# Optimization experiments

Hardware: AMD Instinct MI355X
Metric: run time of the kernel (lower is better)

Reference implementation:

```python
import jax, jax.numpy as jnp
import numpy as np

B = 2048            # reactions per batch
NODES_PER_MOL = 32
N = B * NODES_PER_MOL   # 65536 nodes per slot graph
E = 2 * N               # 131072 edges per slot graph
NODE_IN, EDGE_IN, H = 64, 16, 300
DEPTH = 3


def setup_inputs() -> dict:
    key = jax.random.key(0)
    ks = jax.random.split(key, 24)
    d = {}
    for i, s in enumerate(["r1", "r2", "p1"]):
        d[f"x_{s}"] = jax.random.normal(ks[4 * i], (N, NODE_IN), jnp.float32)
        d[f"e_{s}"] = jax.random.normal(ks[4 * i + 1], (E, EDGE_IN), jnp.float32)
        d[f"src_{s}"] = jax.random.randint(ks[4 * i + 2], (E,), 0, N, jnp.int32)
        d[f"dst_{s}"] = jax.random.randint(ks[4 * i + 3], (E,), 0, N, jnp.int32)
        d[f"seg_{s}"] = jnp.repeat(jnp.arange(B, dtype=jnp.int32), NODES_PER_MOL)
    s = 0.05
    d["Wn"] = jax.random.normal(ks[12], (NODE_IN, H), jnp.float32) * s
    d["bn"] = jnp.zeros((H,), jnp.float32)
    d["We"] = jax.random.normal(ks[13], (EDGE_IN, H), jnp.float32) * s
    d["be"] = jnp.zeros((H,), jnp.float32)
    d["W1"] = jax.random.normal(ks[14], (DEPTH, H, H), jnp.float32) * s
    d["b1"] = jnp.zeros((DEPTH, H), jnp.float32)
    d["W2"] = jax.random.normal(ks[15], (DEPTH, H, H), jnp.float32) * s
    d["b2"] = jnp.zeros((DEPTH, H), jnp.float32)
    return d


def _gin(x, e, src, dst, Wn, bn, We, be, W1, b1, W2, b2):
    # project_node_feats = Linear + ReLU ; project_edge_feats = Linear
    h = jax.nn.relu(x @ Wn + bn)           # [N, H]
    eh = e @ We + be                        # [E, H]
    n = x.shape[0]
    for l in range(DEPTH):
        # GINEConv (eps=0): agg = sum_{j->i} relu(h_j + e_ji); h = MLP(h + agg)
        m = jax.nn.relu(h[src] + eh)        # [E, H]
        agg = jax.ops.segment_sum(m, dst, num_segments=n)
        z = h + agg
        z = jax.nn.relu(z @ W1[l] + b1[l]) @ W2[l] + b2[l]
        if l < DEPTH - 1:
            z = jax.nn.relu(z)              # inter-layer ReLU (dropout = eval no-op)
        h = z
    return h


def reference(x_r1, e_r1, src_r1, dst_r1, seg_r1,
              x_r2, e_r2, src_r2, dst_r2, seg_r2,
              x_p1, e_p1, src_p1, dst_p1, seg_p1,
              Wn, bn, We, be, W1, b1, W2, b2):
    def pooled(x, e, src, dst, seg):
        h = _gin(x, e, src, dst, Wn, bn, We, be, W1, b1, W2, b2)
        # per-molecule sum pooling == the original ragged start:end slice + sum loop
        return jax.ops.segment_sum(h, seg, num_segments=B)   # [B, H]
    reactants = pooled(x_r1, e_r1, src_r1, dst_r1, seg_r1) + \
                pooled(x_r2, e_r2, src_r2, dst_r2, seg_r2)
    products = pooled(x_p1, e_p1, src_p1, dst_p1, seg_p1)
    reaction_feat = reactants - products
    return (reaction_feat, reactants, products)
```

## Files before the change

### kernel.cpp

```cpp
#include <hip/hip_runtime.h>

typedef _Float16 half8 __attribute__((ext_vector_type(8)));
typedef _Float16 half4 __attribute__((ext_vector_type(4)));
typedef float    f32x4 __attribute__((ext_vector_type(4)));

#define N_NODES 65536
#define N_EDGES 131072
#define BB      2048
#define HDIM    300
#define HPAD    320

__global__ __launch_bounds__(256) void prepack_w(const float* __restrict__ src,
                                                 _Float16* __restrict__ dst,
                                                 int Kpad, int Kreal) {
    int idx = blockIdx.x * 256 + threadIdx.x;
    int n = idx / Kpad, k = idx - n * Kpad;
    if (n >= 384) return;
    float v = (n < 300 && k < Kreal) ? src[k * 300 + n] : 0.f;
    dst[idx] = (_Float16)v;
}

__global__ __launch_bounds__(256) void cvt_x(const float* __restrict__ x,
                                             _Float16* __restrict__ xh, int n) {
    int i = blockIdx.x * 256 + threadIdx.x;
    if (i < n) xh[i] = (_Float16)x[i];
}

__global__ __launch_bounds__(256) void cvt_e_csr(const float* __restrict__ ein,
                                                 const int2* __restrict__ se,
                                                 _Float16* __restrict__ ecsr) {
    int i = blockIdx.x * 256 + threadIdx.x;
    if (i >= N_EDGES * 32) return;
    int k = i & 31, s = i >> 5;
    int e = se[s].y;
    ecsr[i] = (_Float16)(k < 16 ? ein[(size_t)e * 16 + k] : 0.f);
}

__device__ __forceinline__ void gload16(const _Float16* g, _Float16* l) {
    __builtin_amdgcn_global_load_lds(
        (const __attribute__((address_space(1))) void*)g,
        (__attribute__((address_space(3))) void*)l, 16, 0, 0);
}

template <bool RELU>
__global__ __launch_bounds__(256) void gemm_f16(
        const _Float16* __restrict__ A,
        const _Float16* __restrict__ Bp, const float* __restrict__ bias,
        _Float16* __restrict__ out, int M, int K) {
    __shared__ _Float16 lds[3][2][128 * 32];

    int bid = blockIdx.x;
    int xcd = bid & 7, grp = bid >> 3;
    int mt = xcd + 8 * (grp / 3);
    int nt = grp % 3;
    int m0 = mt * 128, n0 = nt * 128;
    int t = threadIdx.x;
    int lane = t & 63, w = t >> 6;
    int wr = w >> 1, wc = w & 1;

    int srow[2], sko[2];
    #pragma unroll
    for (int q = 0; q < 2; ++q) {
        int row = (w * 2 + q) * 16 + (lane >> 2);
        int ch = (lane & 3) ^ ((row >> 1) & 3);
        srow[q] = row; sko[q] = ch * 8;
    }

    f32x4 acc[4][4] = {};
    int NK = K >> 5;

    auto stage = [&](int buf, int k0) {
        #pragma unroll
        for (int q = 0; q < 2; ++q) {
            gload16(&A[(size_t)(m0 + srow[q]) * K + k0 + sko[q]], &lds[buf][0][(w * 2 + q) * 512]);
            gload16(&Bp[(size_t)(n0 + srow[q]) * K + k0 + sko[q]], &lds[buf][1][(w * 2 + q) * 512]);
        }
    };

    stage(0, 0);
    if (NK > 1) stage(1, 32);
    for (int kt = 0; kt < NK; ++kt) {
        int cur = kt % 3;
        if (kt + 1 < NK) {
            asm volatile("s_waitcnt vmcnt(4)" ::: "memory");
        } else {
            asm volatile("s_waitcnt vmcnt(0)" ::: "memory");
        }
        __builtin_amdgcn_s_barrier();
        __builtin_amdgcn_sched_barrier(0);
        if (kt + 2 < NK) stage((kt + 2) % 3, (kt + 2) << 5);

        int lr = lane & 15, hi = lane >> 4;
        half8 af[4], bf[4];
        #pragma unroll
        for (int i = 0; i < 4; ++i) {
            int row = wr * 64 + i * 16 + lr;
            int lk = (hi ^ ((row >> 1) & 3)) * 8;
            af[i] = *(const half8*)&lds[cur][0][row * 32 + lk];
        }
        #pragma unroll
        for (int j = 0; j < 4; ++j) {
            int row = wc * 64 + j * 16 + lr;
            int lk = (hi ^ ((row >> 1) & 3)) * 8;
            bf[j] = *(const half8*)&lds[cur][1][row * 32 + lk];
        }
        #pragma unroll
        for (int i = 0; i < 4; ++i)
            #pragma unroll
            for (int j = 0; j < 4; ++j)
                acc[i][j] = __builtin_amdgcn_mfma_f32_16x16x32_f16(af[i], bf[j], acc[i][j], 0, 0, 0);
    }
    __syncthreads();

    _Float16* ct = &lds[0][0][0];
    {
        int lr = lane & 15, lq = (lane >> 4) * 4;
        #pragma unroll
        for (int j = 0; j < 4; ++j) {
            int col = wc * 64 + j * 16 + lr;
            int gcol = n0 + col;
            float bv = (gcol < 300) ? bias[gcol] : 0.f;
            #pragma unroll
            for (int i = 0; i < 4; ++i) {
                int rbase = wr * 64 + i * 16 + lq;
                #pragma unroll
                for (int q = 0; q < 4; ++q) {
                    float v = acc[i][j][q] + bv;
                    if (RELU) v = v > 0.f ? v : 0.f;
                    if (gcol >= 300) v = 0.f;
                    ct[(rbase + q) * 128 + col] = (_Float16)v;
                }
            }
        }
    }
    __syncthreads();
    #pragma unroll
    for (int r = 0; r < 8; ++r) {
        int row = r * 16 + (t >> 4);
        int c8 = (t & 15) * 8;
        if (n0 + c8 < HPAD) {
            half8 v = *(const half8*)&ct[row * 128 + c8];
            *(half8*)&out[(size_t)(m0 + row) * HPAD + n0 + c8] = v;
        }
    }
}

__global__ __launch_bounds__(256) void hist_kernel(const int* __restrict__ dst,
                                                   int* __restrict__ counts) {
    int e = blockIdx.x * 256 + threadIdx.x;
    if (e < N_EDGES) atomicAdd(&counts[dst[e]], 1);
}

__global__ __launch_bounds__(256) void scan_block(const int* __restrict__ in,
                                                  int* __restrict__ partial,
                                                  int* __restrict__ bsum, int nb) {
    __shared__ int s[256];
    int b = blockIdx.x, t = threadIdx.x;
    int v = (b < nb) ? in[b * 256 + t] : 0;
    s[t] = v;
    __syncthreads();
    for (int o = 1; o < 256; o <<= 1) {
        int x = (t >= o) ? s[t - o] : 0;
        __syncthreads();
        s[t] += x;
        __syncthreads();
    }
    partial[b * 256 + t] = s[t] - v;
    if (t == 255 && bsum) bsum[b] = s[255];
}

__global__ __launch_bounds__(256) void add_offsets(const int* __restrict__ partial,
                                                   const int* __restrict__ boff,
                                                   int* __restrict__ rowptr) {
    int i = blockIdx.x * 256 + threadIdx.x;
    if (i < N_NODES) rowptr[i] = partial[i] + boff[i >> 8];
    if (i == 0) rowptr[N_NODES] = N_EDGES;
}

__global__ __launch_bounds__(256) void scatter_csr(const int* __restrict__ src,
                                                   const int* __restrict__ dst,
                                                   const int* __restrict__ rowptr,
                                                   int* __restrict__ cnt,
                                                   int2* __restrict__ se) {
    int e = blockIdx.x * 256 + threadIdx.x;
    if (e >= N_EDGES) return;
    int d = dst[e];
    int pos = atomicAdd(&cnt[d], 1);
    se[rowptr[d] + pos] = make_int2(src[e], e);
}

__global__ __launch_bounds__(320) void gather_z(
        const _Float16* __restrict__ h, const _Float16* __restrict__ ehcsr,
        const int2* __restrict__ se, const int* __restrict__ rowptr,
        _Float16* __restrict__ z, int nblocks) {
    int t = threadIdx.x;
    int c = t % 40, ns = t / 40;
    for (int node = blockIdx.x * 8 + ns; node < N_NODES; node += nblocks * 8) {
        int r0 = rowptr[node], r1 = rowptr[node + 1];
        half8 hn = *(const half8*)&h[(size_t)node * HPAD + c * 8];
        half8 acc = {};
        for (int s = r0; s < r1; s += 4) {
            int nb = r1 - s;
            int idx[4];
            idx[0] = s;
            idx[1] = s + (1 < nb ? 1 : 0);
            idx[2] = s + (2 < nb ? 2 : 0);
            idx[3] = s + (3 < nb ? 3 : 0);
            half8 hv[4], ev[4];
            #pragma unroll
            for (int u = 0; u < 4; ++u) {
                int sp = se[idx[u]].x;
                hv[u] = *(const half8*)&h[(size_t)sp * HPAD + c * 8];
                ev[u] = *(const half8*)&ehcsr[(size_t)idx[u] * HPAD + c * 8];
            }
            #pragma unroll
            for (int u = 0; u < 4; ++u) {
                half8 m = hv[u] + ev[u];
                #pragma unroll
                for (int j = 0; j < 8; ++j)
                    m[j] = m[j] > (_Float16)0 ? m[j] : (_Float16)0;
                if (u < nb) acc += m;
            }
        }
        half8 o = hn + acc;
        *(half8*)&z[(size_t)node * HPAD + c * 8] = o;
    }
}

__global__ __launch_bounds__(128) void pool_kernel(const _Float16* __restrict__ h,
                                                   float* __restrict__ out, int add) {
    int b = blockIdx.x, t = threadIdx.x;
    if (t >= 75) return;
    float a0 = 0, a1 = 0, a2 = 0, a3 = 0;
    for (int r = 0; r < 32; ++r) {
        half4 v = *(const half4*)&h[(size_t)(b * 32 + r) * HPAD + t * 4];
        a0 += (float)v[0]; a1 += (float)v[1]; a2 += (float)v[2]; a3 += (float)v[3];
    }
    f32x4 o = {a0, a1, a2, a3};
    if (add) o += *(f32x4*)&out[b * 300 + t * 4];
    *(f32x4*)&out[b * 300 + t * 4] = o;
}

__global__ __launch_bounds__(256) void diff_kernel(float* __restrict__ reaction,
                                                   const float* __restrict__ reactants,
                                                   const float* __restrict__ products, int n) {
    int i = blockIdx.x * 256 + threadIdx.x;
    if (i < n) reaction[i] = reactants[i] - products[i];
}

extern "C" void kernel_launch(void* const* d_in, const int* in_sizes, int n_in,
                              void* d_out, int out_size, void* d_ws, size_t ws_size,
                              hipStream_t stream) {
    const float* x[3]   = {(const float*)d_in[0], (const float*)d_in[5],  (const float*)d_in[10]};
    const float* ein[3] = {(const float*)d_in[1], (const float*)d_in[6],  (const float*)d_in[11]};
    const int*   src[3] = {(const int*)d_in[2],   (const int*)d_in[7],    (const int*)d_in[12]};
    const int*   dst[3] = {(const int*)d_in[3],   (const int*)d_in[8],    (const int*)d_in[13]};
    const float* Wn = (const float*)d_in[15];
    const float* bn = (const float*)d_in[16];
    const float* We = (const float*)d_in[17];
    const float* be = (const float*)d_in[18];
    const float* W1 = (const float*)d_in[19];
    const float* b1 = (const float*)d_in[20];
    const float* W2 = (const float*)d_in[21];
    const float* b2 = (const float*)d_in[22];

    char* ws = (char*)d_ws;
    size_t off = 0;
    auto alloc = [&](size_t bytes) {
        char* p = ws + off; off += (bytes + 1023) & ~(size_t)1023; return p;
    };
    _Float16* h     = (_Float16*)alloc((size_t)N_NODES * HPAD * 2);
    _Float16* zbuf  = (_Float16*)alloc((size_t)N_NODES * HPAD * 2);
    _Float16* tbuf  = (_Float16*)alloc((size_t)N_NODES * HPAD * 2);
    _Float16* ehcsr = (_Float16*)alloc((size_t)N_EDGES * HPAD * 2);
    int*      counts= (int*)alloc((size_t)N_NODES * 4);
    int*      cnt   = (int*)alloc((size_t)N_NODES * 4);
    int*      part  = (int*)alloc((size_t)N_NODES * 4);
    int*      bsum  = (int*)alloc(256 * 4);
    int*      bpart = (int*)alloc(256 * 4);
    int*      bzero = (int*)alloc(4);
    int*      rowptr= (int*)alloc((size_t)(N_NODES + 1) * 4);
    int2*     se    = (int2*)alloc((size_t)N_EDGES * 8);
    _Float16* Wt1   = (_Float16*)alloc((size_t)3 * 384 * HPAD * 2);
    _Float16* Wt2   = (_Float16*)alloc((size_t)3 * 384 * HPAD * 2);
    _Float16* Wnt   = (_Float16*)alloc((size_t)384 * 64 * 2);
    _Float16* Wet   = (_Float16*)alloc((size_t)384 * 32 * 2);
    _Float16* xh    = (_Float16*)zbuf;
    _Float16* ecsr  = (_Float16*)tbuf;

    if (off > ws_size) return;

    for (int l = 0; l < 3; ++l) {
        prepack_w<<<(384 * HPAD + 255) / 256, 256, 0, stream>>>(W1 + l * 90000, Wt1 + l * 384 * HPAD, HPAD, 300);
        prepack_w<<<(384 * HPAD + 255) / 256, 256, 0, stream>>>(W2 + l * 90000, Wt2 + l * 384 * HPAD, HPAD, 300);
    }
    prepack_w<<<(384 * 64 + 255) / 256, 256, 0, stream>>>(Wn, Wnt, 64, 64);
    prepack_w<<<(384 * 32 + 255) / 256, 256, 0, stream>>>(We, Wet, 32, 16);
    hipMemsetAsync(bzero, 0, 4, stream);

    float* outp      = (float*)d_out;
    float* reaction  = outp;
    float* reactants = outp + (size_t)BB * HDIM;
    float* products  = outp + (size_t)2 * BB * HDIM;

    const int EG = (N_EDGES + 255) / 256;
    for (int g = 0; g < 3; ++g) {
        cvt_x<<<(N_NODES * 64 + 255) / 256, 256, 0, stream>>>(x[g], xh, N_NODES * 64);
        gemm_f16<true><<<512 * 3, 256, 0, stream>>>(xh, Wnt, bn, h, N_NODES, 64);

        hipMemsetAsync(counts, 0, (size_t)2 * N_NODES * 4, stream);
        hist_kernel<<<EG, 256, 0, stream>>>(dst[g], counts);
        scan_block<<<256, 256, 0, stream>>>(counts, part, bsum, 256);
        scan_block<<<1, 256, 0, stream>>>(bsum, bpart, bzero, 1);
        add_offsets<<<256, 256, 0, stream>>>(part, bpart, rowptr);
        scatter_csr<<<EG, 256, 0, stream>>>(src[g], dst[g], rowptr, cnt, se);

        cvt_e_csr<<<(N_EDGES * 32 + 255) / 256, 256, 0, stream>>>(ein[g], se, ecsr);
        gemm_f16<false><<<1024 * 3, 256, 0, stream>>>(ecsr, Wet, be, ehcsr, N_EDGES, 32);

        for (int l = 0; l < 3; ++l) {
            gather_z<<<2048, 320, 0, stream>>>(h, ehcsr, se, rowptr, zbuf, 2048);
            gemm_f16<true><<<512 * 3, 256, 0, stream>>>(zbuf, Wt1 + l * 384 * HPAD, b1 + l * 300, tbuf, N_NODES, HPAD);
            if (l < 2)
                gemm_f16<true ><<<512 * 3, 256, 0, stream>>>(tbuf, Wt2 + l * 384 * HPAD, b2 + l * 300, h, N_NODES, HPAD);
            else
                gemm_f16<false><<<512 * 3, 256, 0, stream>>>(tbuf, Wt2 + l * 384 * HPAD, b2 + l * 300, h, N_NODES, HPAD);
        }
        if (g == 0)      pool_kernel<<<BB, 128, 0, stream>>>(h, reactants, 0);
        else if (g == 1) pool_kernel<<<BB, 128, 0, stream>>>(h, reactants, 1);
        else             pool_kernel<<<BB, 128, 0, stream>>>(h, products, 0);
    }
    diff_kernel<<<((BB * HDIM) + 255) / 256, 256, 0, stream>>>(reaction, reactants, products, BB * HDIM);
}
```

Baseline: 1.098 ms.

## Retile GEMM to 128x160 output tiles with double-buffered LDS

Changes the f16 GEMM output tile from 128x128 (3 N-tiles, the last mostly padding) to 128x160 (2 N-tiles exactly covering the 320 padded columns), giving each wave a 4x5 MFMA accumulator block. The goal is to remove the wasted compute and loads on the padded 384-wide weight rows and to launch fewer blocks. The LDS pipeline moves from triple to double buffering with an extra barrier per K step, and launch bounds request 3 blocks per SM. This raises register use per wave and may weaken load/compute overlap.

```diff
diff --git a/kernel.cpp b/kernel.cpp
--- a/kernel.cpp
+++ b/kernel.cpp
@@ -43,81 +43,86 @@
 }
 
 template <bool RELU>
-__global__ __launch_bounds__(256) void gemm_f16(
+__global__ __launch_bounds__(256, 3) void gemm_f16(
         const _Float16* __restrict__ A,
         const _Float16* __restrict__ Bp, const float* __restrict__ bias,
         _Float16* __restrict__ out, int M, int K) {
-    __shared__ _Float16 lds[3][2][128 * 32];
+    __shared__ _Float16 lds[2][10240];
 
     int bid = blockIdx.x;
     int xcd = bid & 7, grp = bid >> 3;
-    int mt = xcd + 8 * (grp / 3);
-    int nt = grp % 3;
-    int m0 = mt * 128, n0 = nt * 128;
+    int mt = xcd + 8 * (grp >> 1);
+    int nt = grp & 1;
+    int m0 = mt * 128, n0 = nt * 160;
     int t = threadIdx.x;
     int lane = t & 63, w = t >> 6;
-    int wr = w >> 1, wc = w & 1;
-
-    int srow[2], sko[2];
-    #pragma unroll
-    for (int q = 0; q < 2; ++q) {
-        int row = (w * 2 + q) * 16 + (lane >> 2);
-        int ch = (lane & 3) ^ ((row >> 1) & 3);
-        srow[q] = row; sko[q] = ch * 8;
-    }
-
-    f32x4 acc[4][4] = {};
+    int wr = w >> 1, wcn = (w & 1) * 80;
+
+    f32x4 acc[4][5] = {};
     int NK = K >> 5;
 
     auto stage = [&](int buf, int k0) {
         #pragma unroll
         for (int q = 0; q < 2; ++q) {
-            gload16(&A[(size_t)(m0 + srow[q]) * K + k0 + sko[q]], &lds[buf][0][(w * 2 + q) * 512]);
-            gload16(&Bp[(size_t)(n0 + srow[q]) * K + k0 + sko[q]], &lds[buf][1][(w * 2 + q) * 512]);
+            int slot = q * 256 + t;
+            int row = slot >> 2;
+            int ch = ((slot & 3) ^ ((row >> 1) & 3)) << 3;
+            gload16(&A[(size_t)(m0 + row) * K + k0 + ch],
+                    &lds[buf][(q * 256 + w * 64) * 8]);
+        }
+        #pragma unroll
+        for (int q = 0; q < 3; ++q) {
+            int slot = q * 256 + t;
+            int row = slot >> 2;
+            int ch = ((slot & 3) ^ ((row >> 1) & 3)) << 3;
+            gload16(&Bp[(size_t)(n0 + row) * K + k0 + ch],
+                    &lds[buf][4096 + (q * 256 + w * 64) * 8]);
         }
     };
 
     stage(0, 0);
-    if (NK > 1) stage(1, 32);
     for (int kt = 0; kt < NK; ++kt) {
-        int cur = kt % 3;
+        int cur = kt & 1;
         if (kt + 1 < NK) {
-            asm volatile("s_waitcnt vmcnt(4)" ::: "memory");
+            stage(cur ^ 1, (kt + 1) << 5);
+            asm volatile("s_waitcnt vmcnt(5)" ::: "memory");
         } else {
             asm volatile("s_waitcnt vmcnt(0)" ::: "memory");
         }
         __builtin_amdgcn_s_barrier();
         __builtin_amdgcn_sched_barrier(0);
-        if (kt + 2 < NK) stage((kt + 2) % 3, (kt + 2) << 5);
 
         int lr = lane & 15, hi = lane >> 4;
-        half8 af[4], bf[4];
+        half8 af[4], bf[5];
         #pragma unroll
         for (int i = 0; i < 4; ++i) {
             int row = wr * 64 + i * 16 + lr;
             int lk = (hi ^ ((row >> 1) & 3)) * 8;
-            af[i] = *(const half8*)&lds[cur][0][row * 32 + lk];
-        }
-        #pragma unroll
-        for (int j = 0; j < 4; ++j) {
-            int row = wc * 64 + j * 16 + lr;
+            af[i] = *(const half8*)&lds[cur][row * 32 + lk];
+        }
+        #pragma unroll
+        for (int j = 0; j < 5; ++j) {
+            int row = wcn + j * 16 + lr;
             int lk = (hi ^ ((row >> 1) & 3)) * 8;
-            bf[j] = *(const half8*)&lds[cur][1][row * 32 + lk];
+            bf[j] = *(const half8*)&lds[cur][4096 + row * 32 + lk];
         }
         #pragma unroll
         for (int i = 0; i < 4; ++i)
             #pragma unroll
-            for (int j = 0; j < 4; ++j)
+            for (int j = 0; j < 5; ++j)
                 acc[i][j] = __builtin_amdgcn_mfma_f32_16x16x32_f16(af[i], bf[j], acc[i][j], 0, 0, 0);
+
+        __builtin_amdgcn_sched_barrier(0);
+        __builtin_amdgcn_s_barrier();
     }
     __syncthreads();
 
-    _Float16* ct = &lds[0][0][0];
+    _Float16* ct = &lds[0][0];
     {
         int lr = lane & 15, lq = (lane >> 4) * 4;
         #pragma unroll
-        for (int j = 0; j < 4; ++j) {
-            int col = wc * 64 + j * 16 + lr;
+        for (int j = 0; j < 5; ++j) {
+            int col = wcn + j * 16 + lr;
             int gcol = n0 + col;
             float bv = (gcol < 300) ? bias[gcol] : 0.f;
             #pragma unroll
@@ -128,20 +133,18 @@
                     float v = acc[i][j][q] + bv;
                     if (RELU) v = v > 0.f ? v : 0.f;
                     if (gcol >= 300) v = 0.f;
-                    ct[(rbase + q) * 128 + col] = (_Float16)v;
+                    ct[(rbase + q) * 160 + col] = (_Float16)v;
                 }
             }
         }
     }
     __syncthreads();
     #pragma unroll
-    for (int r = 0; r < 8; ++r) {
-        int row = r * 16 + (t >> 4);
-        int c8 = (t & 15) * 8;
-        if (n0 + c8 < HPAD) {
-            half8 v = *(const half8*)&ct[row * 128 + c8];
-            *(half8*)&out[(size_t)(m0 + row) * HPAD + n0 + c8] = v;
-        }
+    for (int r = 0; r < 10; ++r) {
+        int idx = r * 256 + t;
+        int row = idx / 20, c = idx - row * 20;
+        half8 v = *(const half8*)&ct[row * 160 + c * 8];
+        *(half8*)&out[(size_t)(m0 + row) * HPAD + n0 + c * 8] = v;
     }
 }
 
@@ -306,7 +309,7 @@
     const int EG = (N_EDGES + 255) / 256;
     for (int g = 0; g < 3; ++g) {
         cvt_x<<<(N_NODES * 64 + 255) / 256, 256, 0, stream>>>(x[g], xh, N_NODES * 64);
-        gemm_f16<true><<<512 * 3, 256, 0, stream>>>(xh, Wnt, bn, h, N_NODES, 64);
+        gemm_f16<true><<<512 * 2, 256, 0, stream>>>(xh, Wnt, bn, h, N_NODES, 64);
 
         hipMemsetAsync(counts, 0, (size_t)2 * N_NODES * 4, stream);
         hist_kernel<<<EG, 256, 0, stream>>>(dst[g], counts);
@@ -316,15 +319,15 @@
         scatter_csr<<<EG, 256, 0, stream>>>(src[g], dst[g], rowptr, cnt, se);
 
         cvt_e_csr<<<(N_EDGES * 32 + 255) / 256, 256, 0, stream>>>(ein[g], se, ecsr);
-        gemm_f16<false><<<1024 * 3, 256, 0, stream>>>(ecsr, Wet, be, ehcsr, N_EDGES, 32);
+        gemm_f16<false><<<1024 * 2, 256, 0, stream>>>(ecsr, Wet, be, ehcsr, N_EDGES, 32);
 
         for (int l = 0; l < 3; ++l) {
             gather_z<<<2048, 320, 0, stream>>>(h, ehcsr, se, rowptr, zbuf, 2048);
-            gemm_f16<true><<<512 * 3, 256, 0, stream>>>(zbuf, Wt1 + l * 384 * HPAD, b1 + l * 300, tbuf, N_NODES, HPAD);
+            gemm_f16<true><<<512 * 2, 256, 0, stream>>>(zbuf, Wt1 + l * 384 * HPAD, b1 + l * 300, tbuf, N_NODES, HPAD);
             if (l < 2)
-                gemm_f16<true ><<<512 * 3, 256, 0, stream>>>(tbuf, Wt2 + l * 384 * HPAD, b2 + l * 300, h, N_NODES, HPAD);
+                gemm_f16<true ><<<512 * 2, 256, 0, stream>>>(tbuf, Wt2 + l * 384 * HPAD, b2 + l * 300, h, N_NODES, HPAD);
             else
-                gemm_f16<false><<<512 * 3, 256, 0, stream>>>(tbuf, Wt2 + l * 384 * HPAD, b2 + l * 300, h, N_NODES, HPAD);
+                gemm_f16<false><<<512 * 2, 256, 0, stream>>>(tbuf, Wt2 + l * 384 * HPAD, b2 + l * 300, h, N_NODES, HPAD);
         }
         if (g == 0)      pool_kernel<<<BB, 128, 0, stream>>>(h, reactants, 0);
         else if (g == 1) pool_kernel<<<BB, 128, 0, stream>>>(h, reactants, 1);
```

New measurement: 1.043 ms. -5.0%, faster.
